# Performance work log

Measured on AMD Instinct MI355X. Metric: run time of the kernel, lower is better.

Reference implementation:

```python
import jax, jax.numpy as jnp
import numpy as np

CONF = 0.3      # confidence threshold (NMS.conf)
IOU = 0.6       # IoU threshold (NMS.iou)
MAX_WH = 4096.0 # class-offset trick for per-class NMS
K = 2048        # max candidates entering NMS (yolov5-style cap)
MAX_DET = 300   # max detections kept per image (fixed output size)


def setup_inputs() -> dict:
    key = jax.random.key(0)
    kxy, kwh, kobj, kcls = jax.random.split(key, 4)
    B, N, NC = 8, 25200, 80
    # realistic raw predictions: xywh in pixel units for a 640x640 image
    xy = jax.random.uniform(kxy, (B, N, 2), minval=0.0, maxval=640.0)
    wh = jax.random.uniform(kwh, (B, N, 2), minval=2.0, maxval=160.0)
    obj = jax.random.uniform(kobj, (B, N, 1))
    cls = jax.random.uniform(kcls, (B, N, NC))
    x = jnp.concatenate([xy, wh, obj, cls], axis=-1)  # [B, N, 5+NC]
    return {"x": x}


def _xywh2xyxy(b):
    xy, half = b[..., :2], b[..., 2:4] * 0.5
    return jnp.concatenate([xy - half, xy + half], axis=-1)


def _pairwise_iou(boxes):  # boxes: [K, 4] xyxy -> [K, K]
    lt = jnp.maximum(boxes[:, None, :2], boxes[None, :, :2])
    rb = jnp.minimum(boxes[:, None, 2:], boxes[None, :, 2:])
    inter = jnp.clip(rb - lt, 0.0).prod(-1)
    area = (boxes[:, 2] - boxes[:, 0]) * (boxes[:, 3] - boxes[:, 1])
    return inter / (area[:, None] + area[None, :] - inter + 1e-9)


def _nms_single(pred):  # pred: [N, 5+NC]
    obj = pred[:, 4]
    cls_conf = pred[:, 5:] * obj[:, None]          # conf = obj * cls prob
    conf = cls_conf.max(-1)
    cls_id = jnp.argmax(cls_conf, -1)
    valid = (obj > CONF) & (conf > CONF)           # candidate + final threshold
    boxes = _xywh2xyxy(pred[:, :4])
    scores = jnp.where(valid, conf, -1.0)
    top_s, idx = jax.lax.top_k(scores, K)          # cap candidates, sorted desc
    boxes_k = boxes[idx]
    cls_k = cls_id[idx]
    valid_k = top_s > 0.0
    # offset boxes by class so NMS is per-class
    shifted = boxes_k + cls_k[:, None].astype(boxes_k.dtype) * MAX_WH
    iou = _pairwise_iou(shifted)                   # [K, K]
    order = jnp.arange(K)

    def body(keep, i):  # greedy suppression in score order
        active = keep[i] & valid_k[i]
        sup = (iou[i] > IOU) & (order > i)
        keep = jnp.where(active, keep & ~sup, keep)
        return keep, None

    keep, _ = jax.lax.scan(body, jnp.ones((K,), bool), order)
    keep = keep & valid_k
    final_s = jnp.where(keep, top_s, -1.0)
    det_s, det_i = jax.lax.top_k(final_s, MAX_DET)
    dets = jnp.concatenate(
        [boxes_k[det_i], top_s[det_i][:, None],
         cls_k[det_i][:, None].astype(boxes_k.dtype)], axis=-1)  # [MAX_DET, 6]
    return dets, det_s > 0.0


def reference(x):
    # returns (dets [B, MAX_DET, 6] = xyxy,conf,cls ; valid mask [B, MAX_DET])
    return jax.vmap(_nms_single)(x)
```

## Files before the change

kernel.cpp:

```cpp
#include <hip/hip_runtime.h>
#include <hip/hip_bf16.h>

#define B 8
#define N 25200
#define ROW 85
#define NC 80
#define K 2048
#define MAXDET 300
#define NBUCKET 16384
#define CAND_CAP 4096
#define NCHUNK 32
#define STILE 64

__global__ void __launch_bounds__(256)
nms_score_kernel(const float* __restrict__ x,
                 float* __restrict__ scores,
                 int* __restrict__ cls_id,
                 unsigned* __restrict__ hist,
                 float4* __restrict__ boxes4) {
    int b = blockIdx.y;
    int i0 = blockIdx.x * STILE;
    int rows = N - i0; if (rows > STILE) rows = STILE;
    __shared__ float lx[STILE * ROW];
    {
        const float4* s4 = (const float4*)(x + ((size_t)b * N + i0) * ROW);
        float4* d4 = (float4*)lx;
        int nv = rows * ROW / 4;
        for (int k = threadIdx.x; k < nv; k += 256) d4[k] = s4[k];
    }
    __syncthreads();
    int g = threadIdx.x >> 2;
    int q = threadIdx.x & 3;
    if (g >= rows) return;
    const float* p = lx + g * ROW;
    float obj = p[4];
    float best = -1e30f;
    int bc = 127;
    if (obj > 0.3f) {
        #pragma unroll
        for (int k = 0; k < 20; ++k) {
            int c = q + 4 * k;
            float v = __fmul_rn(p[5 + c], obj);
            if (v > best) { best = v; bc = c; }
        }
    }
    #pragma unroll
    for (int m = 1; m < 4; m <<= 1) {
        float ov = __shfl_xor(best, m, 64);
        int   oc = __shfl_xor(bc, m, 64);
        if (ov > best || (ov == best && oc < bc)) { best = ov; bc = oc; }
    }
    if (q == 0) {
        int i = i0 + g;
        float score = (obj > 0.3f && best > 0.3f) ? best : -1.0f;
        scores[b * N + i] = score;
        cls_id[b * N + i] = (bc == 127) ? 0 : bc;
        float cx = p[0], cy = p[1], w = p[2], h = p[3];
        float hx = __fmul_rn(w, 0.5f);
        float hy = __fmul_rn(h, 0.5f);
        boxes4[b * N + i] = make_float4(__fsub_rn(cx, hx), __fsub_rn(cy, hy),
                                        __fadd_rn(cx, hx), __fadd_rn(cy, hy));
        if (score > 0.0f) {
            int qb = (int)(__fmul_rn(score, 16384.0f));
            if (qb > NBUCKET - 1) qb = NBUCKET - 1;
            atomicAdd(&hist[b * NBUCKET + qb], 1u);
        }
    }
}

__global__ void __launch_bounds__(1024, 1)
nms_select_kernel(const float* __restrict__ scores,
                  const float4* __restrict__ boxes4,
                  const int* __restrict__ cls_id,
                  const unsigned* __restrict__ hist,
                  float* __restrict__ top_s,
                  float* __restrict__ boxes,
                  int* __restrict__ clsk,
                  float* __restrict__ shifted,
                  float* __restrict__ area,
                  unsigned long long* __restrict__ keepbits,
                  unsigned long long* __restrict__ gclsmask) {
    __shared__ unsigned loff[NBUCKET];
    __shared__ unsigned lcnt16[NBUCKET / 2];
    __shared__ unsigned long long lk[CAND_CAP];
    __shared__ unsigned long long lcm[NC * NCHUNK];
    __shared__ unsigned wsum[16];

    int b = blockIdx.x;
    int t = threadIdx.x;
    int ln = t & 63, wv = t >> 6;
    constexpr int NITER = (N + 1023) / 1024;

    if (t < NCHUNK) keepbits[b * NCHUNK + t] = 0ULL;

    {
        uint4 z = {0u, 0u, 0u, 0u};
        uint4* d2 = (uint4*)lcnt16;
        for (int k = t; k < NBUCKET / 8; k += 1024) d2[k] = z;
    }
    for (int k = t; k < CAND_CAP; k += 1024) lk[k] = 0ULL;
    for (int k = t; k < NC * NCHUNK; k += 1024) lcm[k] = 0ULL;

    unsigned v[16];
    unsigned A4 = (unsigned)(NBUCKET - 16 - t * 16) / 4;
    {
        const uint4* gh = (const uint4*)(hist + (size_t)b * NBUCKET);
        uint4 u0 = gh[A4 + 0];
        uint4 u1 = gh[A4 + 1];
        uint4 u2 = gh[A4 + 2];
        uint4 u3 = gh[A4 + 3];
        unsigned u[16] = {u0.x,u0.y,u0.z,u0.w, u1.x,u1.y,u1.z,u1.w,
                          u2.x,u2.y,u2.z,u2.w, u3.x,u3.y,u3.z,u3.w};
        #pragma unroll
        for (int k = 0; k < 16; ++k) v[k] = u[15 - k];
    }
    unsigned S = 0;
    #pragma unroll
    for (int k = 0; k < 16; ++k) S += v[k];
    unsigned pref = S;
    #pragma unroll
    for (int o = 1; o < 64; o <<= 1) { unsigned u = __shfl_up(pref, o, 64); if (ln >= o) pref += u; }
    if (ln == 63) wsum[wv] = pref;
    __syncthreads();
    unsigned wbase = 0;
    for (int w = 0; w < wv; ++w) wbase += wsum[w];
    unsigned running = wbase + pref - S;
    {
        unsigned o[16];
        #pragma unroll
        for (int k = 0; k < 16; ++k) { o[15 - k] = running; running += v[k]; }
        ((uint4*)loff)[A4 + 0] = make_uint4(o[0],  o[1],  o[2],  o[3]);
        ((uint4*)loff)[A4 + 1] = make_uint4(o[4],  o[5],  o[6],  o[7]);
        ((uint4*)loff)[A4 + 2] = make_uint4(o[8],  o[9],  o[10], o[11]);
        ((uint4*)loff)[A4 + 3] = make_uint4(o[12], o[13], o[14], o[15]);
    }
    __syncthreads();

    float sreg[NITER];
    #pragma unroll
    for (int r = 0; r < NITER; ++r) {
        int i = t + r * 1024;
        sreg[r] = (i < N) ? scores[b * N + i] : -1.0f;
    }
    #pragma unroll
    for (int r = 0; r < NITER; ++r) {
        float s = sreg[r];
        if (s > 0.0f) {
            int i = t + r * 1024;
            int q = (int)(__fmul_rn(s, 16384.0f));
            if (q > NBUCKET - 1) q = NBUCKET - 1;
            unsigned start = loff[q];
            if (start < CAND_CAP) {
                unsigned sh = (q & 1) * 16;
                unsigned old = atomicAdd(&lcnt16[q >> 1], 1u << sh);
                unsigned rank = (old >> sh) & 0xFFFFu;
                unsigned pos = start + rank;
                if (pos < CAND_CAP) {
                    unsigned long long key =
                        ((unsigned long long)__float_as_uint(s) << 32) | (unsigned)(~i);
                    lk[pos] = key;
                }
            }
        }
    }
    __syncthreads();

    for (int q = t; q < NBUCKET; q += 1024) {
        unsigned start = loff[q];
        if (start < CAND_CAP) {
            unsigned c = (lcnt16[q >> 1] >> ((q & 1) * 16)) & 0xFFFFu;
            unsigned m = c;
            if (m > CAND_CAP - start) m = CAND_CAP - start;
            if (m >= 2) {
                for (unsigned a = start + 1; a < start + m; ++a) {
                    unsigned long long kv = lk[a];
                    unsigned p2 = a;
                    while (p2 > start && lk[p2 - 1] < kv) { lk[p2] = lk[p2 - 1]; --p2; }
                    lk[p2] = kv;
                }
            }
        }
    }
    __syncthreads();

    for (int r = t; r < K; r += 1024) {
        unsigned long long key = lk[r];
        float s;
        int idx;
        float x1, y1, x2, y2;
        int c;
        if (key == 0ULL) {
            s = -1.0f; x1 = y1 = x2 = y2 = 0.0f; c = 0;
        } else {
            s = __uint_as_float((unsigned)(key >> 32));
            idx = (int)(~(unsigned)key);
            float4 bb = boxes4[(size_t)b * N + idx];
            x1 = bb.x; y1 = bb.y; x2 = bb.z; y2 = bb.w;
            c = cls_id[b * N + idx];
            atomicOr(&lcm[c * NCHUNK + (r >> 6)], 1ULL << (r & 63));
        }
        int o = b * K + r;
        top_s[o] = s;
        boxes[o * 4 + 0] = x1; boxes[o * 4 + 1] = y1;
        boxes[o * 4 + 2] = x2; boxes[o * 4 + 3] = y2;
        clsk[o] = c;
        float sh = __fmul_rn((float)c, 4096.0f);
        float sx1 = __fadd_rn(x1, sh), sy1 = __fadd_rn(y1, sh);
        float sx2 = __fadd_rn(x2, sh), sy2 = __fadd_rn(y2, sh);
        shifted[o * 4 + 0] = sx1; shifted[o * 4 + 1] = sy1;
        shifted[o * 4 + 2] = sx2; shifted[o * 4 + 3] = sy2;
        area[o] = __fmul_rn(__fsub_rn(sx2, sx1), __fsub_rn(sy2, sy1));
    }
    __syncthreads();
    for (int k = t; k < NC * NCHUNK; k += 1024)
        gclsmask[(size_t)b * NC * NCHUNK + k] = lcm[k];
}

__global__ void __launch_bounds__(64)
nms_classout_kernel(const unsigned long long* __restrict__ gclsmask,
                    const float* __restrict__ top_s,
                    const int* __restrict__ clsk,
                    const float* __restrict__ shifted,
                    const float* __restrict__ area,
                    const float* __restrict__ boxes,
                    unsigned long long* __restrict__ keepbits,
                    unsigned* __restrict__ done_ctr,
                    float* __restrict__ out) {
    int c = blockIdx.x, b = blockIdx.y;
    int t = threadIdx.x;
    unsigned long long below = (t == 0) ? 0ULL : (~0ULL >> (64 - t));

    __shared__ int srank[K];
    __shared__ unsigned long long skeep[NCHUNK];

    const unsigned long long* cm = gclsmask + ((size_t)b * NC + c) * NCHUNK;
    int n = 0;
    #pragma unroll 4
    for (int ch = 0; ch < NCHUNK; ++ch) {
        unsigned long long m = cm[ch];
        if ((m >> t) & 1ULL) srank[n + __popcll(m & below)] = ch * 64 + t;
        n += __popcll(m);
    }
    __syncthreads();

    if (n > 0 && n <= 64) {
        float x1 = 0.f, y1 = 0.f, x2 = 0.f, y2 = 0.f, ar = 0.f;
        int r = -1;
        if (t < n) {
            r = srank[t];
            const float* sb = shifted + ((size_t)b * K + r) * 4;
            x1 = sb[0]; y1 = sb[1]; x2 = sb[2]; y2 = sb[3];
            ar = area[b * K + r];
        }
        unsigned long long keepw = (n == 64) ? ~0ULL : ((1ULL << n) - 1ULL);
        for (int i = 0; i < n; ++i) {
            if (!((keepw >> i) & 1ULL)) continue;
            float bx1 = __shfl(x1, i, 64), by1 = __shfl(y1, i, 64);
            float bx2 = __shfl(x2, i, 64), by2 = __shfl(y2, i, 64);
            float ba  = __shfl(ar, i, 64);
            bool cond = false;
            if (t > i && t < n) {
                float lx = fmaxf(bx1, x1), ly = fmaxf(by1, y1);
                float rx = fminf(bx2, x2), ry = fminf(by2, y2);
                float w = fmaxf(__fsub_rn(rx, lx), 0.0f);
                float h = fmaxf(__fsub_rn(ry, ly), 0.0f);
                float inter = __fmul_rn(w, h);
                float denom = __fadd_rn(__fsub_rn(__fadd_rn(ba, ar), inter), 1e-9f);
                cond = __fdiv_rn(inter, denom) > 0.6f;
            }
            keepw &= ~__ballot(cond);
        }
        if (t < n && ((keepw >> t) & 1ULL))
            atomicOr(&keepbits[b * NCHUNK + (r >> 6)], 1ULL << (r & 63));
    } else if (n > 64) {
        for (int w = t; w < NCHUNK; w += 64) {
            int lo = w * 64;
            unsigned long long vw;
            if (n >= lo + 64)      vw = ~0ULL;
            else if (n <= lo)      vw = 0ULL;
            else                   vw = (1ULL << (n - lo)) - 1ULL;
            skeep[w] = vw;
        }
        __syncthreads();
        for (int i = 0; i < n; ++i) {
            if (!((skeep[i >> 6] >> (i & 63)) & 1ULL)) continue;
            int ri = srank[i];
            const float* sbi = shifted + ((size_t)b * K + ri) * 4;
            float bx1 = sbi[0], by1 = sbi[1], bx2 = sbi[2], by2 = sbi[3];
            float ba = area[b * K + ri];
            int jb_hi = (n - 1) >> 6;
            for (int jb2 = (i + 1) >> 6; jb2 <= jb_hi; ++jb2) {
                int j = jb2 * 64 + t;
                bool cond = false;
                if (j > i && j < n) {
                    int rj = srank[j];
                    const float* sbj = shifted + ((size_t)b * K + rj) * 4;
                    float x1 = sbj[0], y1 = sbj[1], x2 = sbj[2], y2 = sbj[3];
                    float arj = area[b * K + rj];
                    float lx = fmaxf(bx1, x1), ly = fmaxf(by1, y1);
                    float rx = fminf(bx2, x2), ry = fminf(by2, y2);
                    float w = fmaxf(__fsub_rn(rx, lx), 0.0f);
                    float h = fmaxf(__fsub_rn(ry, ly), 0.0f);
                    float inter = __fmul_rn(w, h);
                    float denom = __fadd_rn(__fsub_rn(__fadd_rn(ba, arj), inter), 1e-9f);
                    cond = __fdiv_rn(inter, denom) > 0.6f;
                }
                unsigned long long sup = __ballot(cond);
                if (t == 0) skeep[jb2] &= ~sup;
            }
            __syncthreads();
        }
        for (int j = t; j < n; j += 64) {
            if ((skeep[j >> 6] >> (j & 63)) & 1ULL) {
                int r = srank[j];
                atomicOr(&keepbits[b * NCHUNK + (r >> 6)], 1ULL << (r & 63));
            }
        }
    }

    __threadfence();
    unsigned old = 0;
    if (t == 0) old = atomicAdd(&done_ctr[b], 1u);
    old = (unsigned)__shfl((int)old, 0, 64);
    if (old == NC - 1) {
        __threadfence();
        __shared__ unsigned long long kept[NCHUNK];
        if (t < NCHUNK)
            kept[t] = atomicOr(&keepbits[b * NCHUNK + t], 0ULL);
        __syncthreads();

        int total = 0;
        for (int ch = 0; ch < NCHUNK; ++ch) total += __popcll(kept[ch]);

        float* dets  = out + (size_t)b * MAXDET * 6;
        float* flags = out + (size_t)B * MAXDET * 6 + (size_t)b * MAXDET;
        int kc = 0, nc2 = 0;
        for (int ch = 0; ch < NCHUNK; ++ch) {
            int i = ch * 64 + t;
            unsigned long long m = kept[ch];
            bool k = ((m >> t) & 1ULL) != 0ULL;
            int pc = __popcll(m);
            int slot = k ? (kc + __popcll(m & below))
                         : (total + nc2 + __popcll((~m) & below));
            if (slot < MAXDET) {
                int o = b * K + i;
                dets[slot * 6 + 0] = boxes[o * 4 + 0];
                dets[slot * 6 + 1] = boxes[o * 4 + 1];
                dets[slot * 6 + 2] = boxes[o * 4 + 2];
                dets[slot * 6 + 3] = boxes[o * 4 + 3];
                dets[slot * 6 + 4] = top_s[o];
                dets[slot * 6 + 5] = (float)clsk[o];
                flags[slot] = k ? 1.0f : 0.0f;
            }
            kc += pc;
            nc2 += 64 - pc;
        }
    }
}

extern "C" void kernel_launch(void* const* d_in, const int* in_sizes, int n_in,
                              void* d_out, int out_size, void* d_ws, size_t ws_size,
                              hipStream_t stream) {
    const float* x = (const float*)d_in[0];
    float* out = (float*)d_out;

    char* ws = (char*)d_ws;
    size_t off = 0;
    auto alloc = [&](size_t bytes) -> void* {
        void* p = ws + off;
        off += bytes;
        off = (off + 255) & ~(size_t)255;
        return p;
    };

    float*    scores = (float*)    alloc((size_t)B * N * 4);
    int*      cls_id = (int*)      alloc((size_t)B * N * 4);
    float4*   boxes4 = (float4*)   alloc((size_t)B * N * 16);
    float*    top_s  = (float*)    alloc((size_t)B * K * 4);
    float*    boxes  = (float*)    alloc((size_t)B * K * 4 * 4);
    int*      clsk   = (int*)      alloc((size_t)B * K * 4);
    float*    shifted= (float*)    alloc((size_t)B * K * 4 * 4);
    float*    area   = (float*)    alloc((size_t)B * K * 4);
    unsigned long long* keepbits = (unsigned long long*) alloc((size_t)B * NCHUNK * 8);
    unsigned long long* gclsmask = (unsigned long long*) alloc((size_t)B * NC * NCHUNK * 8);
    unsigned* hist     = (unsigned*) alloc((size_t)B * NBUCKET * 4);
    unsigned* done_ctr = (unsigned*) alloc(256);
    (void)ws_size;

    hipMemsetAsync(hist, 0, (size_t)B * NBUCKET * 4 + 256, stream);
    nms_score_kernel<<<dim3((N + STILE - 1) / STILE, B), 256, 0, stream>>>(
        x, scores, cls_id, hist, boxes4);
    nms_select_kernel<<<B, 1024, 0, stream>>>(scores, boxes4, cls_id, hist,
                                              top_s, boxes, clsk, shifted, area,
                                              keepbits, gclsmask);
    nms_classout_kernel<<<dim3(NC, B), 64, 0, stream>>>(gclsmask, top_s, clsk,
                                                        shifted, area, boxes,
                                                        keepbits, done_ctr, out);
}
```

Before: 142.7 us.

## Fuse select and per-class NMS into one kernel with ready-flag handoff

```diff
diff --git a/kernel.cpp b/kernel.cpp
--- a/kernel.cpp
+++ b/kernel.cpp
@@ -1,5 +1,4 @@
 #include <hip/hip_runtime.h>
-#include <hip/hip_bf16.h>
 
 #define B 8
 #define N 25200
@@ -11,15 +10,21 @@
 #define CAND_CAP 4096
 #define NCHUNK 32
 #define STILE 64
+#define CTR_STRIDE 64
 
 __global__ void __launch_bounds__(256)
 nms_score_kernel(const float* __restrict__ x,
                  float* __restrict__ scores,
                  int* __restrict__ cls_id,
-                 unsigned* __restrict__ hist,
-                 float4* __restrict__ boxes4) {
+                 float4* __restrict__ boxes4,
+                 unsigned* __restrict__ ready,
+                 unsigned* __restrict__ done_ctr) {
     int b = blockIdx.y;
     int i0 = blockIdx.x * STILE;
+    if (blockIdx.x == 0 && threadIdx.x == 0) {
+        ready[b * CTR_STRIDE] = 0u;
+        done_ctr[b * CTR_STRIDE] = 0u;
+    }
     int rows = N - i0; if (rows > STILE) rows = STILE;
     __shared__ float lx[STILE * ROW];
     {
@@ -60,194 +65,210 @@
         float hy = __fmul_rn(h, 0.5f);
         boxes4[b * N + i] = make_float4(__fsub_rn(cx, hx), __fsub_rn(cy, hy),
                                         __fadd_rn(cx, hx), __fadd_rn(cy, hy));
-        if (score > 0.0f) {
-            int qb = (int)(__fmul_rn(score, 16384.0f));
-            if (qb > NBUCKET - 1) qb = NBUCKET - 1;
-            atomicAdd(&hist[b * NBUCKET + qb], 1u);
-        }
     }
 }
 
 __global__ void __launch_bounds__(1024, 1)
-nms_select_kernel(const float* __restrict__ scores,
-                  const float4* __restrict__ boxes4,
-                  const int* __restrict__ cls_id,
-                  const unsigned* __restrict__ hist,
-                  float* __restrict__ top_s,
-                  float* __restrict__ boxes,
-                  int* __restrict__ clsk,
-                  float* __restrict__ shifted,
-                  float* __restrict__ area,
-                  unsigned long long* __restrict__ keepbits,
-                  unsigned long long* __restrict__ gclsmask) {
+nms_tail_kernel(const float* __restrict__ scores,
+                const float4* __restrict__ boxes4,
+                const int* __restrict__ cls_id,
+                float* __restrict__ top_s,
+                float* __restrict__ boxes,
+                int* __restrict__ clsk,
+                float* __restrict__ shifted,
+                float* __restrict__ area,
+                unsigned long long* __restrict__ keepbits,
+                unsigned long long* __restrict__ gclsmask,
+                unsigned* __restrict__ ready,
+                unsigned* __restrict__ done_ctr,
+                float* __restrict__ out) {
     __shared__ unsigned loff[NBUCKET];
     __shared__ unsigned lcnt16[NBUCKET / 2];
     __shared__ unsigned long long lk[CAND_CAP];
     __shared__ unsigned long long lcm[NC * NCHUNK];
     __shared__ unsigned wsum[16];
 
-    int b = blockIdx.x;
+    int bid = blockIdx.x;
     int t = threadIdx.x;
     int ln = t & 63, wv = t >> 6;
-    constexpr int NITER = (N + 1023) / 1024;
-
-    if (t < NCHUNK) keepbits[b * NCHUNK + t] = 0ULL;
-
-    {
-        uint4 z = {0u, 0u, 0u, 0u};
-        uint4* d2 = (uint4*)lcnt16;
-        for (int k = t; k < NBUCKET / 8; k += 1024) d2[k] = z;
-    }
-    for (int k = t; k < CAND_CAP; k += 1024) lk[k] = 0ULL;
-    for (int k = t; k < NC * NCHUNK; k += 1024) lcm[k] = 0ULL;
-
-    unsigned v[16];
-    unsigned A4 = (unsigned)(NBUCKET - 16 - t * 16) / 4;
-    {
-        const uint4* gh = (const uint4*)(hist + (size_t)b * NBUCKET);
-        uint4 u0 = gh[A4 + 0];
-        uint4 u1 = gh[A4 + 1];
-        uint4 u2 = gh[A4 + 2];
-        uint4 u3 = gh[A4 + 3];
-        unsigned u[16] = {u0.x,u0.y,u0.z,u0.w, u1.x,u1.y,u1.z,u1.w,
-                          u2.x,u2.y,u2.z,u2.w, u3.x,u3.y,u3.z,u3.w};
+    unsigned long long below = (ln == 0) ? 0ULL : (~0ULL >> (64 - ln));
+
+    if (bid < B) {
+        int b = bid;
+        constexpr int NITER = (N + 1023) / 1024;
+
+        if (t < NCHUNK) keepbits[b * NCHUNK + t] = 0ULL;
+        {
+            uint4 z = {0u, 0u, 0u, 0u};
+            uint4* d1 = (uint4*)loff;
+            for (int k = t; k < NBUCKET / 4; k += 1024) d1[k] = z;
+            uint4* d2 = (uint4*)lcnt16;
+            for (int k = t; k < NBUCKET / 8; k += 1024) d2[k] = z;
+        }
+        for (int k = t; k < CAND_CAP; k += 1024) lk[k] = 0ULL;
+        for (int k = t; k < NC * NCHUNK; k += 1024) lcm[k] = 0ULL;
+        __syncthreads();
+
+        float sreg[NITER];
         #pragma unroll
-        for (int k = 0; k < 16; ++k) v[k] = u[15 - k];
-    }
-    unsigned S = 0;
-    #pragma unroll
-    for (int k = 0; k < 16; ++k) S += v[k];
-    unsigned pref = S;
-    #pragma unroll
-    for (int o = 1; o < 64; o <<= 1) { unsigned u = __shfl_up(pref, o, 64); if (ln >= o) pref += u; }
-    if (ln == 63) wsum[wv] = pref;
-    __syncthreads();
-    unsigned wbase = 0;
-    for (int w = 0; w < wv; ++w) wbase += wsum[w];
-    unsigned running = wbase + pref - S;
-    {
-        unsigned o[16];
+        for (int r = 0; r < NITER; ++r) {
+            int i = t + r * 1024;
+            float s = (i < N) ? scores[b * N + i] : -1.0f;
+            sreg[r] = s;
+            if (s > 0.0f) {
+                int q = (int)(__fmul_rn(s, 16384.0f));
+                if (q > NBUCKET - 1) q = NBUCKET - 1;
+                atomicAdd(&loff[q], 1u);
+            }
+        }
+        __syncthreads();
+
+        unsigned v[16];
+        unsigned A4 = (unsigned)(NBUCKET - 16 - t * 16) / 4;
+        {
+            uint4 u0 = ((uint4*)loff)[A4 + 0];
+            uint4 u1 = ((uint4*)loff)[A4 + 1];
+            uint4 u2 = ((uint4*)loff)[A4 + 2];
+            uint4 u3 = ((uint4*)loff)[A4 + 3];
+            unsigned u[16] = {u0.x,u0.y,u0.z,u0.w, u1.x,u1.y,u1.z,u1.w,
+                              u2.x,u2.y,u2.z,u2.w, u3.x,u3.y,u3.z,u3.w};
+            #pragma unroll
+            for (int k = 0; k < 16; ++k) v[k] = u[15 - k];
+        }
+        unsigned S = 0;
         #pragma unroll
-        for (int k = 0; k < 16; ++k) { o[15 - k] = running; running += v[k]; }
-        ((uint4*)loff)[A4 + 0] = make_uint4(o[0],  o[1],  o[2],  o[3]);
-        ((uint4*)loff)[A4 + 1] = make_uint4(o[4],  o[5],  o[6],  o[7]);
-        ((uint4*)loff)[A4 + 2] = make_uint4(o[8],  o[9],  o[10], o[11]);
-        ((uint4*)loff)[A4 + 3] = make_uint4(o[12], o[13], o[14], o[15]);
-    }
-    __syncthreads();
-
-    float sreg[NITER];
-    #pragma unroll
-    for (int r = 0; r < NITER; ++r) {
-        int i = t + r * 1024;
-        sreg[r] = (i < N) ? scores[b * N + i] : -1.0f;
-    }
-    #pragma unroll
-    for (int r = 0; r < NITER; ++r) {
-        float s = sreg[r];
-        if (s > 0.0f) {
-            int i = t + r * 1024;
-            int q = (int)(__fmul_rn(s, 16384.0f));
-            if (q > NBUCKET - 1) q = NBUCKET - 1;
+        for (int k = 0; k < 16; ++k) S += v[k];
+        unsigned pref = S;
+        #pragma unroll
+        for (int o = 1; o < 64; o <<= 1) { unsigned u = __shfl_up(pref, o, 64); if (ln >= o) pref += u; }
+        if (ln == 63) wsum[wv] = pref;
+        __syncthreads();
+        unsigned wbase = 0;
+        for (int w = 0; w < wv; ++w) wbase += wsum[w];
+        unsigned running = wbase + pref - S;
+        {
+            unsigned o[16];
+            #pragma unroll
+            for (int k = 0; k < 16; ++k) { o[15 - k] = running; running += v[k]; }
+            ((uint4*)loff)[A4 + 0] = make_uint4(o[0],  o[1],  o[2],  o[3]);
+            ((uint4*)loff)[A4 + 1] = make_uint4(o[4],  o[5],  o[6],  o[7]);
+            ((uint4*)loff)[A4 + 2] = make_uint4(o[8],  o[9],  o[10], o[11]);
+            ((uint4*)loff)[A4 + 3] = make_uint4(o[12], o[13], o[14], o[15]);
+        }
+        __syncthreads();
+
+        #pragma unroll
+        for (int r = 0; r < NITER; ++r) {
+            float s = sreg[r];
+            if (s > 0.0f) {
+                int i = t + r * 1024;
+                int q = (int)(__fmul_rn(s, 16384.0f));
+                if (q > NBUCKET - 1) q = NBUCKET - 1;
+                unsigned start = loff[q];
+                if (start < CAND_CAP) {
+                    unsigned sh = (q & 1) * 16;
+                    unsigned old = atomicAdd(&lcnt16[q >> 1], 1u << sh);
+                    unsigned rank = (old >> sh) & 0xFFFFu;
+                    unsigned pos = start + rank;
+                    if (pos < CAND_CAP) {
+                        unsigned long long key =
+                            ((unsigned long long)__float_as_uint(s) << 32) | (unsigned)(~i);
+                        lk[pos] = key;
+                    }
+                }
+            }
+        }
+        __syncthreads();
+
+        for (int q = t; q < NBUCKET; q += 1024) {
             unsigned start = loff[q];
             if (start < CAND_CAP) {
-                unsigned sh = (q & 1) * 16;
-                unsigned old = atomicAdd(&lcnt16[q >> 1], 1u << sh);
-                unsigned rank = (old >> sh) & 0xFFFFu;
-                unsigned pos = start + rank;
-                if (pos < CAND_CAP) {
-                    unsigned long long key =
-                        ((unsigned long long)__float_as_uint(s) << 32) | (unsigned)(~i);
-                    lk[pos] = key;
+                unsigned c = (lcnt16[q >> 1] >> ((q & 1) * 16)) & 0xFFFFu;
+                unsigned m = c;
+                if (m > CAND_CAP - start) m = CAND_CAP - start;
+                if (m >= 2) {
+                    for (unsigned a = start + 1; a < start + m; ++a) {
+                        unsigned long long kv = lk[a];
+                        unsigned p2 = a;
+                        while (p2 > start && lk[p2 - 1] < kv) { lk[p2] = lk[p2 - 1]; --p2; }
+                        lk[p2] = kv;
+                    }
                 }
             }
         }
+        __syncthreads();
+
+        for (int r = t; r < K; r += 1024) {
+            unsigned long long key = lk[r];
+            float s;
+            int idx;
+            float x1, y1, x2, y2;
+            int c;
+            if (key == 0ULL) {
+                s = -1.0f; x1 = y1 = x2 = y2 = 0.0f; c = 0;
+            } else {
+                s = __uint_as_float((unsigned)(key >> 32));
+                idx = (int)(~(unsigned)key);
+                float4 bb = boxes4[(size_t)b * N + idx];
+                x1 = bb.x; y1 = bb.y; x2 = bb.z; y2 = bb.w;
+                c = cls_id[b * N + idx];
+                atomicOr(&lcm[c * NCHUNK + (r >> 6)], 1ULL << (r & 63));
+            }
+            int o = b * K + r;
+            top_s[o] = s;
+            boxes[o * 4 + 0] = x1; boxes[o * 4 + 1] = y1;
+            boxes[o * 4 + 2] = x2; boxes[o * 4 + 3] = y2;
+            clsk[o] = c;
+            float sh = __fmul_rn((float)c, 4096.0f);
+            float sx1 = __fadd_rn(x1, sh), sy1 = __fadd_rn(y1, sh);
+            float sx2 = __fadd_rn(x2, sh), sy2 = __fadd_rn(y2, sh);
+            shifted[o * 4 + 0] = sx1; shifted[o * 4 + 1] = sy1;
+            shifted[o * 4 + 2] = sx2; shifted[o * 4 + 3] = sy2;
+            area[o] = __fmul_rn(__fsub_rn(sx2, sx1), __fsub_rn(sy2, sy1));
+        }
+        __syncthreads();
+        for (int k = t; k < NC * NCHUNK; k += 1024)
+            gclsmask[(size_t)b * NC * NCHUNK + k] = lcm[k];
+        __syncthreads();
+        if (t == 0) {
+            __threadfence();
+            atomicExch(&ready[b * CTR_STRIDE], 1u);
+        }
+        return;
+    }
+
+    int gid = bid - B;
+    int b = gid / 5;
+    int grp = gid % 5;
+    int c = grp * 16 + wv;
+
+    if (t == 0) {
+        while (atomicOr(&ready[b * CTR_STRIDE], 0u) == 0u)
+            __builtin_amdgcn_s_sleep(8);
+        __threadfence();
     }
     __syncthreads();
 
-    for (int q = t; q < NBUCKET; q += 1024) {
-        unsigned start = loff[q];
-        if (start < CAND_CAP) {
-            unsigned c = (lcnt16[q >> 1] >> ((q & 1) * 16)) & 0xFFFFu;
-            unsigned m = c;
-            if (m > CAND_CAP - start) m = CAND_CAP - start;
-            if (m >= 2) {
-                for (unsigned a = start + 1; a < start + m; ++a) {
-                    unsigned long long kv = lk[a];
-                    unsigned p2 = a;
-                    while (p2 > start && lk[p2 - 1] < kv) { lk[p2] = lk[p2 - 1]; --p2; }
-                    lk[p2] = kv;
-                }
-            }
-        }
-    }
-    __syncthreads();
-
-    for (int r = t; r < K; r += 1024) {
-        unsigned long long key = lk[r];
-        float s;
-        int idx;
-        float x1, y1, x2, y2;
-        int c;
-        if (key == 0ULL) {
-            s = -1.0f; x1 = y1 = x2 = y2 = 0.0f; c = 0;
-        } else {
-            s = __uint_as_float((unsigned)(key >> 32));
-            idx = (int)(~(unsigned)key);
-            float4 bb = boxes4[(size_t)b * N + idx];
-            x1 = bb.x; y1 = bb.y; x2 = bb.z; y2 = bb.w;
-            c = cls_id[b * N + idx];
-            atomicOr(&lcm[c * NCHUNK + (r >> 6)], 1ULL << (r & 63));
-        }
-        int o = b * K + r;
-        top_s[o] = s;
-        boxes[o * 4 + 0] = x1; boxes[o * 4 + 1] = y1;
-        boxes[o * 4 + 2] = x2; boxes[o * 4 + 3] = y2;
-        clsk[o] = c;
-        float sh = __fmul_rn((float)c, 4096.0f);
-        float sx1 = __fadd_rn(x1, sh), sy1 = __fadd_rn(y1, sh);
-        float sx2 = __fadd_rn(x2, sh), sy2 = __fadd_rn(y2, sh);
-        shifted[o * 4 + 0] = sx1; shifted[o * 4 + 1] = sy1;
-        shifted[o * 4 + 2] = sx2; shifted[o * 4 + 3] = sy2;
-        area[o] = __fmul_rn(__fsub_rn(sx2, sx1), __fsub_rn(sy2, sy1));
-    }
-    __syncthreads();
-    for (int k = t; k < NC * NCHUNK; k += 1024)
-        gclsmask[(size_t)b * NC * NCHUNK + k] = lcm[k];
-}
-
-__global__ void __launch_bounds__(64)
-nms_classout_kernel(const unsigned long long* __restrict__ gclsmask,
-                    const float* __restrict__ top_s,
-                    const int* __restrict__ clsk,
-                    const float* __restrict__ shifted,
-                    const float* __restrict__ area,
-                    const float* __restrict__ boxes,
-                    unsigned long long* __restrict__ keepbits,
-                    unsigned* __restrict__ done_ctr,
-                    float* __restrict__ out) {
-    int c = blockIdx.x, b = blockIdx.y;
-    int t = threadIdx.x;
-    unsigned long long below = (t == 0) ? 0ULL : (~0ULL >> (64 - t));
-
-    __shared__ int srank[K];
-    __shared__ unsigned long long skeep[NCHUNK];
-
     const unsigned long long* cm = gclsmask + ((size_t)b * NC + c) * NCHUNK;
-    int n = 0;
-    #pragma unroll 4
+    unsigned long long membw = 0ULL;
+    int n = 0, r = -1, ch_i = -1, myk = -1;
+    unsigned long long mych = 0ULL;
     for (int ch = 0; ch < NCHUNK; ++ch) {
         unsigned long long m = cm[ch];
-        if ((m >> t) & 1ULL) srank[n + __popcll(m & below)] = ch * 64 + t;
-        n += __popcll(m);
-    }
-    __syncthreads();
+        if (ln == ch) membw = m;
+        int cnt = __popcll(m);
+        if (myk < 0 && ln < n + cnt) { mych = m; myk = ln - n; ch_i = ch; }
+        n += cnt;
+    }
+    if (myk >= 0) {
+        unsigned long long mm = mych;
+        for (int z = 0; z < myk; ++z) mm &= mm - 1;
+        r = ch_i * 64 + __builtin_ctzll(mm);
+    }
 
     if (n > 0 && n <= 64) {
         float x1 = 0.f, y1 = 0.f, x2 = 0.f, y2 = 0.f, ar = 0.f;
-        int r = -1;
-        if (t < n) {
-            r = srank[t];
+        if (ln < n) {
             const float* sb = shifted + ((size_t)b * K + r) * 4;
             x1 = sb[0]; y1 = sb[1]; x2 = sb[2]; y2 = sb[3];
             ar = area[b * K + r];
@@ -259,7 +280,7 @@
             float bx2 = __shfl(x2, i, 64), by2 = __shfl(y2, i, 64);
             float ba  = __shfl(ar, i, 64);
             bool cond = false;
-            if (t > i && t < n) {
+            if (ln > i && ln < n) {
                 float lx = fmaxf(bx1, x1), ly = fmaxf(by1, y1);
                 float rx = fminf(bx2, x2), ry = fminf(by2, y2);
                 float w = fmaxf(__fsub_rn(rx, lx), 0.0f);
@@ -270,33 +291,27 @@
             }
             keepw &= ~__ballot(cond);
         }
-        if (t < n && ((keepw >> t) & 1ULL))
+        if (ln < n && ((keepw >> ln) & 1ULL))
             atomicOr(&keepbits[b * NCHUNK + (r >> 6)], 1ULL << (r & 63));
     } else if (n > 64) {
-        for (int w = t; w < NCHUNK; w += 64) {
-            int lo = w * 64;
-            unsigned long long vw;
-            if (n >= lo + 64)      vw = ~0ULL;
-            else if (n <= lo)      vw = 0ULL;
-            else                   vw = (1ULL << (n - lo)) - 1ULL;
-            skeep[w] = vw;
-        }
-        __syncthreads();
-        for (int i = 0; i < n; ++i) {
-            if (!((skeep[i >> 6] >> (i & 63)) & 1ULL)) continue;
-            int ri = srank[i];
-            const float* sbi = shifted + ((size_t)b * K + ri) * 4;
+        unsigned long long keepw2 = membw;
+        for (int i = 0; i < K; ++i) {
+            int ch = i >> 6;
+            unsigned long long mw = __shfl(membw, ch, 64);
+            unsigned long long kw = __shfl(keepw2, ch, 64);
+            unsigned long long bi = 1ULL << (i & 63);
+            if (!(mw & kw & bi)) continue;
+            const float* sbi = shifted + ((size_t)b * K + i) * 4;
             float bx1 = sbi[0], by1 = sbi[1], bx2 = sbi[2], by2 = sbi[3];
-            float ba = area[b * K + ri];
-            int jb_hi = (n - 1) >> 6;
-            for (int jb2 = (i + 1) >> 6; jb2 <= jb_hi; ++jb2) {
-                int j = jb2 * 64 + t;
+            float ba = area[b * K + i];
+            for (int c2 = ch; c2 < NCHUNK; ++c2) {
+                int j = c2 * 64 + ln;
+                unsigned long long mw2 = __shfl(membw, c2, 64);
                 bool cond = false;
-                if (j > i && j < n) {
-                    int rj = srank[j];
-                    const float* sbj = shifted + ((size_t)b * K + rj) * 4;
+                if (j > i && ((mw2 >> ln) & 1ULL)) {
+                    const float* sbj = shifted + ((size_t)b * K + j) * 4;
                     float x1 = sbj[0], y1 = sbj[1], x2 = sbj[2], y2 = sbj[3];
-                    float arj = area[b * K + rj];
+                    float arj = area[b * K + j];
                     float lx = fmaxf(bx1, x1), ly = fmaxf(by1, y1);
                     float rx = fminf(bx2, x2), ry = fminf(by2, y2);
                     float w = fmaxf(__fsub_rn(rx, lx), 0.0f);
@@ -306,39 +321,31 @@
                     cond = __fdiv_rn(inter, denom) > 0.6f;
                 }
                 unsigned long long sup = __ballot(cond);
-                if (t == 0) skeep[jb2] &= ~sup;
-            }
-            __syncthreads();
-        }
-        for (int j = t; j < n; j += 64) {
-            if ((skeep[j >> 6] >> (j & 63)) & 1ULL) {
-                int r = srank[j];
-                atomicOr(&keepbits[b * NCHUNK + (r >> 6)], 1ULL << (r & 63));
-            }
-        }
+                if (ln == c2) keepw2 &= ~sup;
+            }
+        }
+        if (ln < NCHUNK && (keepw2 & membw))
+            atomicOr(&keepbits[b * NCHUNK + ln], keepw2 & membw);
     }
 
     __threadfence();
     unsigned old = 0;
-    if (t == 0) old = atomicAdd(&done_ctr[b], 1u);
+    if (ln == 0) old = atomicAdd(&done_ctr[b * CTR_STRIDE], 1u);
     old = (unsigned)__shfl((int)old, 0, 64);
     if (old == NC - 1) {
         __threadfence();
-        __shared__ unsigned long long kept[NCHUNK];
-        if (t < NCHUNK)
-            kept[t] = atomicOr(&keepbits[b * NCHUNK + t], 0ULL);
-        __syncthreads();
-
+        unsigned long long kw = 0ULL;
+        if (ln < NCHUNK) kw = atomicOr(&keepbits[b * NCHUNK + ln], 0ULL);
         int total = 0;
-        for (int ch = 0; ch < NCHUNK; ++ch) total += __popcll(kept[ch]);
+        for (int ch = 0; ch < NCHUNK; ++ch) total += __popcll(__shfl(kw, ch, 64));
 
         float* dets  = out + (size_t)b * MAXDET * 6;
         float* flags = out + (size_t)B * MAXDET * 6 + (size_t)b * MAXDET;
         int kc = 0, nc2 = 0;
         for (int ch = 0; ch < NCHUNK; ++ch) {
-            int i = ch * 64 + t;
-            unsigned long long m = kept[ch];
-            bool k = ((m >> t) & 1ULL) != 0ULL;
+            int i = ch * 64 + ln;
+            unsigned long long m = __shfl(kw, ch, 64);
+            bool k = ((m >> ln) & 1ULL) != 0ULL;
             int pc = __popcll(m);
             int slot = k ? (kc + __popcll(m & below))
                          : (total + nc2 + __popcll((~m) & below));
@@ -383,17 +390,13 @@
     float*    area   = (float*)    alloc((size_t)B * K * 4);
     unsigned long long* keepbits = (unsigned long long*) alloc((size_t)B * NCHUNK * 8);
     unsigned long long* gclsmask = (unsigned long long*) alloc((size_t)B * NC * NCHUNK * 8);
-    unsigned* hist     = (unsigned*) alloc((size_t)B * NBUCKET * 4);
-    unsigned* done_ctr = (unsigned*) alloc(256);
+    unsigned* ready    = (unsigned*) alloc((size_t)B * CTR_STRIDE * 4);
+    unsigned* done_ctr = (unsigned*) alloc((size_t)B * CTR_STRIDE * 4);
     (void)ws_size;
 
-    hipMemsetAsync(hist, 0, (size_t)B * NBUCKET * 4 + 256, stream);
     nms_score_kernel<<<dim3((N + STILE - 1) / STILE, B), 256, 0, stream>>>(
-        x, scores, cls_id, hist, boxes4);
-    nms_select_kernel<<<B, 1024, 0, stream>>>(scores, boxes4, cls_id, hist,
-                                              top_s, boxes, clsk, shifted, area,
-                                              keepbits, gclsmask);
-    nms_classout_kernel<<<dim3(NC, B), 64, 0, stream>>>(gclsmask, top_s, clsk,
-                                                        shifted, area, boxes,
-                                                        keepbits, done_ctr, out);
+        x, scores, cls_id, boxes4, ready, done_ctr);
+    nms_tail_kernel<<<B + 5 * B, 1024, 0, stream>>>(
+        scores, boxes4, cls_id, top_s, boxes, clsk, shifted, area,
+        keepbits, gclsmask, ready, done_ctr, out);
 }
```

Measured after the change: 141.9 us. No clear change (-0.5%).
